# Optimization experiments

Measured on AMD Instinct MI355X. Metric: run time of the kernel, lower is better.

## Reference

```python
import jax, jax.numpy as jnp
import numpy as np

MUL = 64                  # multiplicity of 0e and 1o channels
N_NODES = 50000
N_EDGES = 500000
DIM_KEY = 32
FEAT = MUL * 4            # 64x0e (64) + 64x1o (192) = 256
# e3nn FullyConnectedTensorProduct(in, '10x0e', out) normalization:
# path_weight * w3j = 1/sqrt(mul_in * mul_z) = 1/sqrt(64*10)
INV640 = 1.0 / np.sqrt(MUL * 10)
ISQ3 = 1.0 / np.sqrt(3.0)   # w3j(1,1,0) = delta/sqrt(3)
ISQ2 = 1.0 / np.sqrt(2.0)   # path_weight sqrt(alpha) after 'element' norm (2 paths/out)


def _fctp(x, z, W0, W1):
    """FullyConnectedTensorProduct('64x0e+64x1o', '10x0e', '64x0e+64x1o').
    Scalars mix 0e block, vectors mix 1o block; w3j/path-weight factors reduce to 1/sqrt(640)."""
    x0 = x[:, :MUL]                       # (N, 64)
    x1 = x[:, MUL:].reshape(-1, MUL, 3)   # (N, 64, 3)
    o0 = jnp.einsum('nu,nv,uvw->nw', x0, z, W0) * INV640
    o1 = jnp.einsum('nuk,nv,uvw->nwk', x1, z, W1) * INV640
    return jnp.concatenate([o0, o1.reshape(-1, MUL * 3)], axis=-1)


def setup_inputs() -> dict:
    key = jax.random.key(0)
    ks = jax.random.split(key, 13)
    return {
        'x': jax.random.normal(ks[0], (N_NODES, FEAT), jnp.float32),
        'z': jax.random.normal(ks[1], (N_NODES, 10), jnp.float32),
        'edge_src': jax.random.randint(ks[2], (N_EDGES,), 0, N_NODES, jnp.int32),
        'edge_dst': jax.random.randint(ks[3], (N_EDGES,), 0, N_NODES, jnp.int32),
        'edge_len_emb': jax.random.normal(ks[4], (N_EDGES, DIM_KEY), jnp.float32),
        'edge_attr': jax.random.normal(ks[5], (N_EDGES, 4), jnp.float32),
        # learned params: four FCTPs (si, lin1, lin2 each have one 0e and one 1o path)
        'W_si0': jax.random.normal(ks[6], (MUL, 10, MUL), jnp.float32),
        'W_si1': jax.random.normal(ks[7], (MUL, 10, MUL), jnp.float32),
        'W_l1_0': jax.random.normal(ks[8], (MUL, 10, MUL), jnp.float32),
        'W_l1_1': jax.random.normal(ks[9], (MUL, 10, MUL), jnp.float32),
        'W_l2_0': jax.random.normal(ks[10], (MUL, 10, MUL), jnp.float32),
        'W_l2_1': jax.random.normal(ks[11], (MUL, 10, MUL), jnp.float32),
        # per-edge TP weights: 4 'uvu' paths x 64 = 256
        'tp_weight': jax.random.normal(ks[12], (DIM_KEY, 4 * MUL), jnp.float32),
    }


def reference(x, z, edge_src, edge_dst, edge_len_emb, edge_attr,
              W_si0, W_si1, W_l1_0, W_l1_1, W_l2_0, W_l2_1, tp_weight):
    n = x.shape[0]
    s = _fctp(x, z, W_si0, W_si1)          # self-interaction
    xl = _fctp(x, z, W_l1_0, W_l1_1)       # lin1

    w = edge_len_emb @ tp_weight           # (E, 256) per-edge TP weights
    w1, w2, w3, w4 = jnp.split(w, 4, axis=-1)  # instr order: 0ex0e->0e, 0ex1o->1o, 1ox0e->1o, 1ox1o->0e

    xs = xl[edge_src]                      # gather (E, 256)
    x0 = xs[:, :MUL]                       # (E, 64)
    x1 = xs[:, MUL:].reshape(-1, MUL, 3)   # (E, 64, 3)
    sh0 = edge_attr[:, 0:1]                # (E, 1) scalar SH
    sh1 = edge_attr[:, 1:4]                # (E, 3) vector SH

    # 'uvu' weighted tensor product (component norm, element path norm):
    # out_0e = sqrt(1/2) * [ w1*x0*sh0 + w4*(x1.sh1)/sqrt(3) ]
    e0 = ISQ2 * (w1 * x0 * sh0 + ISQ3 * w4 * jnp.einsum('euk,ek->eu', x1, sh1))
    # out_1o = sqrt(3/2)/sqrt(3) * [ w2*x0*sh1 + w3*x1*sh0 ]
    e1 = ISQ2 * (w2[:, :, None] * x0[:, :, None] * sh1[:, None, :]
                 + w3[:, :, None] * x1 * sh0[:, :, None])
    edge_out = jnp.concatenate([e0, e1.reshape(-1, MUL * 3)], axis=-1)  # (E, 256)

    # scatter-add messages to destination nodes
    agg = jnp.zeros((n, FEAT), edge_out.dtype).at[edge_dst].add(edge_out)

    x_out = _fctp(agg, z, W_l2_0, W_l2_1)  # lin2
    return s + x_out / 10
```

## Files before the change

### kernel.cpp

```cpp
#include <hip/hip_runtime.h>

#define MULT 64
#define FEATD 256
#define ZDIM 10

#define INV640f 0.03952847075210474f
#define ISQ2f   0.7071067811865476f
#define ISQ3f   0.5773502691896258f

typedef _Float16 f16_t;
typedef f16_t f16x8_t __attribute__((ext_vector_type(8)));
typedef f16_t f16x4_t __attribute__((ext_vector_type(4)));
typedef float f32x4_t __attribute__((ext_vector_type(4)));

__global__ __launch_bounds__(256) void transform_x2(
    const float* __restrict__ x, f16_t* __restrict__ Xs,
    f16_t* __restrict__ Xv, int N)
{
    int idx = blockIdx.x * 256 + threadIdx.x;
    if (idx >= N * MULT) return;
    int n = idx >> 6;
    int u = idx & 63;
    const float* row = x + (size_t)n * FEATD;
    Xs[idx] = (f16_t)row[u];
    const float* x1p = row + MULT + u * 3;
    Xv[((size_t)3 * n + 0) * MULT + u] = (f16_t)x1p[0];
    Xv[((size_t)3 * n + 1) * MULT + u] = (f16_t)x1p[1];
    Xv[((size_t)3 * n + 2) * MULT + u] = (f16_t)x1p[2];
}

__device__ __forceinline__ void preload_W(
    const float* __restrict__ W, int c0, int q, int mm, f16x8_t (&B)[20])
{
    const int col = c0 + mm;
#pragma unroll
    for (int ks = 0; ks < 20; ++ks) {
        const int v = ks >> 1;
        const int ub = ((ks & 1) << 5) + (q << 3);
        const int base = v * 64 + col;
#pragma unroll
        for (int j = 0; j < 8; ++j)
            B[ks][j] = (f16_t)W[(ub + j) * 640 + base];
    }
}

__global__ __launch_bounds__(256, 2) void fctp_stageA_mfma(
    const f16_t* __restrict__ Xs, const f16_t* __restrict__ Xv,
    const float* __restrict__ z,
    const float* __restrict__ Wsi0, const float* __restrict__ Wsi1,
    const float* __restrict__ Wl10, const float* __restrict__ Wl11,
    float* __restrict__ out, f16_t* __restrict__ xls,
    f16_t* __restrict__ xlv, int N)
{
    const int lane = threadIdx.x & 63;
    const int wave = threadIdx.x >> 6;
    const int c0 = wave << 4;
    const int q = lane >> 4;
    const int mm = lane & 15;
    const bool sc = (int)blockIdx.x < 128;
    const float* WA = sc ? Wsi0 : Wsi1;
    const float* WB = sc ? Wl10 : Wl11;
    const f16_t* Xsel = sc ? Xs : Xv;
    const int ntiles = sc ? (N >> 4) : ((3 * N) >> 4);
    const int worker = sc ? (int)blockIdx.x : ((int)blockIdx.x - 128);
    const int nworkers = sc ? 128 : 384;

    f16x8_t BA[20], BB[20];
    preload_W(WA, c0, q, mm, BA);
    preload_W(WB, c0, q, mm, BB);

    for (int tile = worker; tile < ntiles; tile += nworkers) {
        const int r = (tile << 4) + mm;
        f16x8_t xlo = *(const f16x8_t*)(Xsel + ((size_t)r << 6) + (q << 3));
        f16x8_t xhi = *(const f16x8_t*)(Xsel + ((size_t)r << 6) + 32 + (q << 3));
        float xf[16];
#pragma unroll
        for (int j = 0; j < 8; ++j) { xf[j] = (float)xlo[j]; xf[8 + j] = (float)xhi[j]; }
        const unsigned node = sc ? (unsigned)r : ((unsigned)r / 3u);
        float zr[ZDIM];
#pragma unroll
        for (int v = 0; v < ZDIM; ++v) zr[v] = z[(size_t)node * ZDIM + v] * INV640f;

        f32x4_t accA = {0.f, 0.f, 0.f, 0.f}, accB = {0.f, 0.f, 0.f, 0.f};
#pragma unroll
        for (int ks = 0; ks < 20; ++ks) {
            const float zv = zr[ks >> 1];
            const int xo = (ks & 1) << 3;
            f16x8_t af;
#pragma unroll
            for (int j = 0; j < 8; ++j) af[j] = (f16_t)(zv * xf[xo + j]);
            accA = __builtin_amdgcn_mfma_f32_16x16x32_f16(af, BA[ks], accA, 0, 0, 0);
            accB = __builtin_amdgcn_mfma_f32_16x16x32_f16(af, BB[ks], accB, 0, 0, 0);
        }

        const int w = c0 + mm;
        const int rb = (tile << 4) + (q << 2);
#pragma unroll
        for (int reg = 0; reg < 4; ++reg) {
            const int ro = rb + reg;
            if (sc) {
                out[(size_t)ro * FEATD + w] = accA[reg];
                xls[((size_t)ro << 6) + w] = (f16_t)accB[reg];
            } else {
                const unsigned nn = (unsigned)ro / 3u;
                const int k = ro - 3 * (int)nn;
                out[(size_t)nn * FEATD + MULT + w * 3 + k] = accA[reg];
                xlv[((size_t)ro << 6) + w] = (f16_t)accB[reg];
            }
        }
    }
}

__global__ __launch_bounds__(256, 2) void fctp_stageC_mfma(
    const float* __restrict__ aggs, const float* __restrict__ aggv,
    const float* __restrict__ z,
    const float* __restrict__ Wl20, const float* __restrict__ Wl21,
    float* __restrict__ out, int N)
{
    const int lane = threadIdx.x & 63;
    const int wave = threadIdx.x >> 6;
    const int c0 = wave << 4;
    const int q = lane >> 4;
    const int mm = lane & 15;
    const bool sc = (int)blockIdx.x < 128;
    const float* W = sc ? Wl20 : Wl21;
    const float* Asel = sc ? aggs : aggv;
    const int ntiles = sc ? (N >> 4) : ((3 * N) >> 4);
    const int worker = sc ? (int)blockIdx.x : ((int)blockIdx.x - 128);
    const int nworkers = sc ? 128 : 384;

    f16x8_t B[20];
    preload_W(W, c0, q, mm, B);

    for (int tile = worker; tile < ntiles; tile += nworkers) {
        const int r = (tile << 4) + mm;
        const float* ap = Asel + ((size_t)r << 6) + (q << 3);
        float4 l0 = *(const float4*)(ap);
        float4 l1 = *(const float4*)(ap + 4);
        float4 h0 = *(const float4*)(ap + 32);
        float4 h1 = *(const float4*)(ap + 36);
        float xf[16] = {l0.x, l0.y, l0.z, l0.w, l1.x, l1.y, l1.z, l1.w,
                        h0.x, h0.y, h0.z, h0.w, h1.x, h1.y, h1.z, h1.w};
        const unsigned node = sc ? (unsigned)r : ((unsigned)r / 3u);
        float zr[ZDIM];
#pragma unroll
        for (int v = 0; v < ZDIM; ++v)
            zr[v] = z[(size_t)node * ZDIM + v] * (INV640f * 0.1f);

        f32x4_t acc = {0.f, 0.f, 0.f, 0.f};
#pragma unroll
        for (int ks = 0; ks < 20; ++ks) {
            const float zv = zr[ks >> 1];
            const int xo = (ks & 1) << 3;
            f16x8_t af;
#pragma unroll
            for (int j = 0; j < 8; ++j) af[j] = (f16_t)(zv * xf[xo + j]);
            acc = __builtin_amdgcn_mfma_f32_16x16x32_f16(af, B[ks], acc, 0, 0, 0);
        }

        const int w = c0 + mm;
        const int rb = (tile << 4) + (q << 2);
#pragma unroll
        for (int reg = 0; reg < 4; ++reg) {
            const int ro = rb + reg;
            size_t idx;
            if (sc) {
                idx = (size_t)ro * FEATD + w;
            } else {
                const unsigned nn = (unsigned)ro / 3u;
                const int k = ro - 3 * (int)nn;
                idx = (size_t)nn * FEATD + MULT + w * 3 + k;
            }
            out[idx] = out[idx] + acc[reg];
        }
    }
}

__global__ __launch_bounds__(256) void hist_kernel(
    const int* __restrict__ edst, int* __restrict__ cnt, int E)
{
    int e = blockIdx.x * 256 + threadIdx.x;
    if (e >= E) return;
    atomicAdd(&cnt[edst[e]], 1);
}

__global__ __launch_bounds__(1024) void scan_block(
    const int* __restrict__ cnt, int* __restrict__ off,
    int* __restrict__ bsum, int N)
{
    __shared__ int sh[1024];
    int tid = threadIdx.x;
    int i = blockIdx.x * 1024 + tid;
    int v = (i < N) ? cnt[i] : 0;
    sh[tid] = v;
    __syncthreads();
#pragma unroll
    for (int d = 1; d < 1024; d <<= 1) {
        int t = (tid >= d) ? sh[tid - d] : 0;
        __syncthreads();
        sh[tid] += t;
        __syncthreads();
    }
    if (i < N) off[i + 1] = sh[tid];
    if (tid == 1023) bsum[blockIdx.x] = sh[1023];
    if (i == 0) off[0] = 0;
}

__global__ __launch_bounds__(64) void scan_sums(int* __restrict__ bsum, int nb)
{
    int tid = threadIdx.x;
    int v = (tid < nb) ? bsum[tid] : 0;
#pragma unroll
    for (int d = 1; d < 64; d <<= 1) {
        int t = __shfl_up(v, d, 64);
        if (tid >= d) v += t;
    }
    int ex = __shfl_up(v, 1, 64);
    if (tid == 0) ex = 0;
    if (tid < nb) bsum[tid] = ex;
}

__global__ __launch_bounds__(1024) void scan_add(
    int* __restrict__ off, const int* __restrict__ bsum, int N)
{
    int i = blockIdx.x * 1024 + threadIdx.x;
    if (i < N) off[i + 1] += bsum[blockIdx.x];
}

__global__ __launch_bounds__(256) void scatter_kernel(
    const int* __restrict__ edst, const int* __restrict__ esrc,
    const float* __restrict__ eattr, const int* __restrict__ off,
    int* __restrict__ cursor, int* __restrict__ perm,
    int* __restrict__ sperm, float* __restrict__ eattr_p, int E)
{
    int e = blockIdx.x * 256 + threadIdx.x;
    if (e >= E) return;
    int d = edst[e];
    int pos = off[d] + atomicAdd(&cursor[d], 1);
    perm[pos] = e;
    sperm[pos] = esrc[e];
    float4 at = *(const float4*)(eattr + (size_t)e * 4);
    *(float4*)(eattr_p + (size_t)pos * 4) = at;
}

__global__ __launch_bounds__(256, 2) void wgemm_kernel(
    const int* __restrict__ perm, const float* __restrict__ elem,
    const float* __restrict__ tpw, f16_t* __restrict__ wbuf,
    int lo, int ntiles)
{
    int tt = blockIdx.x * 4 + (threadIdx.x >> 6);
    if (tt >= ntiles) return;
    const int lane = threadIdx.x & 63;
    const int mm = lane & 15, q = lane >> 4;

    f16x8_t B[16];
#pragma unroll
    for (int s = 0; s < 16; ++s)
#pragma unroll
        for (int j = 0; j < 8; ++j)
            B[s][j] = (f16_t)tpw[(q * 8 + j) * 256 + s * 16 + mm];

    int p = lo + tt * 16 + mm;
    int e = perm[p];
    const float* er = elem + ((size_t)e << 5) + q * 8;
    float4 ea = *(const float4*)er;
    float4 eb = *(const float4*)(er + 4);
    f16x8_t A;
    A[0] = (f16_t)ea.x; A[1] = (f16_t)ea.y; A[2] = (f16_t)ea.z; A[3] = (f16_t)ea.w;
    A[4] = (f16_t)eb.x; A[5] = (f16_t)eb.y; A[6] = (f16_t)eb.z; A[7] = (f16_t)eb.w;

    f32x4_t D[16];
#pragma unroll
    for (int s = 0; s < 16; ++s) {
        f32x4_t zer = {0.f, 0.f, 0.f, 0.f};
        D[s] = __builtin_amdgcn_mfma_f32_16x16x32_f16(A, B[s], zer, 0, 0, 0);
    }

#pragma unroll
    for (int reg = 0; reg < 4; ++reg) {
        const int row = q * 4 + reg;
        const size_t base = ((size_t)(tt * 16 + row)) << 6;
#pragma unroll
        for (int t = 0; t < 4; ++t) {
            const int u = t * 16 + mm;
            f16x4_t wq;
            wq[0] = (f16_t)(D[0 * 4 + t][reg] * ISQ2f);
            wq[1] = (f16_t)(D[1 * 4 + t][reg] * ISQ2f);
            wq[2] = (f16_t)(D[2 * 4 + t][reg] * ISQ2f);
            wq[3] = (f16_t)(D[3 * 4 + t][reg] * (ISQ2f * ISQ3f));
            *(f16x4_t*)(wbuf + ((base + u) << 2)) = wq;
        }
    }
}

__device__ __forceinline__ void agg_edge5(
    float xs, float v0, float v1, float v2, int i, int lo,
    const f16_t* __restrict__ wbuf, const float* __restrict__ eattr_p, int u,
    float& accx, float& accy, float& accz, float& accw)
{
    f16x4_t wq = *(const f16x4_t*)(wbuf + ((((size_t)(i - lo)) << 6) + u) * 4);
    float w1 = (float)wq[0], w2 = (float)wq[1], w3 = (float)wq[2], w4 = (float)wq[3];
    float4 at = *(const float4*)(eattr_p + ((size_t)i << 2));
    float dot3 = v0 * at.y + v1 * at.z + v2 * at.w;
    accx = fmaf(w1 * xs, at.x, accx);
    accx = fmaf(w4, dot3, accx);
    float w2x = w2 * xs;
    accy = fmaf(w2x, at.y, accy);
    accz = fmaf(w2x, at.z, accz);
    accw = fmaf(w2x, at.w, accw);
    float w3s = w3 * at.x;
    accy = fmaf(w3s, v0, accy);
    accz = fmaf(w3s, v1, accz);
    accw = fmaf(w3s, v2, accw);
}

__global__ __launch_bounds__(256, 8) void aggregate5(
    const int* __restrict__ off, const int* __restrict__ sperm,
    const f16_t* __restrict__ wbuf, const float* __restrict__ eattr_p,
    const f16_t* __restrict__ xls, const f16_t* __restrict__ xlv,
    float* __restrict__ aggs, float* __restrict__ aggv,
    int N, int lo, int hi)
{
    int n = (blockIdx.x * 256 + threadIdx.x) >> 6;
    if (n >= N) return;
    int u = threadIdx.x & 63;

    int s0 = __builtin_amdgcn_readfirstlane(off[n]);
    int s1 = __builtin_amdgcn_readfirstlane(off[n + 1]);
    int cs0 = s0 > lo ? s0 : lo;
    int cs1 = s1 < hi ? s1 : hi;
    if (cs0 >= cs1) return;

    float accx = 0.f, accy = 0.f, accz = 0.f, accw = 0.f;
    const int last = cs1 - 1;

    int sa = __builtin_amdgcn_readfirstlane(sperm[cs0]);
    float a_xs = (float)xls[((size_t)sa << 6) + u];
    float a_v0 = (float)xlv[((size_t)(3 * sa + 0) << 6) + u];
    float a_v1 = (float)xlv[((size_t)(3 * sa + 1) << 6) + u];
    float a_v2 = (float)xlv[((size_t)(3 * sa + 2) << 6) + u];
    int ib = (cs0 + 1 <= last) ? cs0 + 1 : last;
    int sb = __builtin_amdgcn_readfirstlane(sperm[ib]);
    float b_xs = (float)xls[((size_t)sb << 6) + u];
    float b_v0 = (float)xlv[((size_t)(3 * sb + 0) << 6) + u];
    float b_v1 = (float)xlv[((size_t)(3 * sb + 1) << 6) + u];
    float b_v2 = (float)xlv[((size_t)(3 * sb + 2) << 6) + u];

    int i = cs0;
    while (true) {
        agg_edge5(a_xs, a_v0, a_v1, a_v2, i, lo, wbuf, eattr_p, u,
                  accx, accy, accz, accw);
        {
            int inx = (i + 2 <= last) ? i + 2 : last;
            int sn = __builtin_amdgcn_readfirstlane(sperm[inx]);
            a_xs = (float)xls[((size_t)sn << 6) + u];
            a_v0 = (float)xlv[((size_t)(3 * sn + 0) << 6) + u];
            a_v1 = (float)xlv[((size_t)(3 * sn + 1) << 6) + u];
            a_v2 = (float)xlv[((size_t)(3 * sn + 2) << 6) + u];
        }
        if (++i > last) break;
        agg_edge5(b_xs, b_v0, b_v1, b_v2, i, lo, wbuf, eattr_p, u,
                  accx, accy, accz, accw);
        {
            int inx = (i + 2 <= last) ? i + 2 : last;
            int sn = __builtin_amdgcn_readfirstlane(sperm[inx]);
            b_xs = (float)xls[((size_t)sn << 6) + u];
            b_v0 = (float)xlv[((size_t)(3 * sn + 0) << 6) + u];
            b_v1 = (float)xlv[((size_t)(3 * sn + 1) << 6) + u];
            b_v2 = (float)xlv[((size_t)(3 * sn + 2) << 6) + u];
        }
        if (++i > last) break;
    }

    aggs[((size_t)n << 6) + u] += accx;
    aggv[((size_t)(3 * n + 0) << 6) + u] += accy;
    aggv[((size_t)(3 * n + 1) << 6) + u] += accz;
    aggv[((size_t)(3 * n + 2) << 6) + u] += accw;
}

extern "C" void kernel_launch(void* const* d_in, const int* in_sizes, int n_in,
                              void* d_out, int out_size, void* d_ws, size_t ws_size,
                              hipStream_t stream)
{
    const float* x     = (const float*)d_in[0];
    const float* z     = (const float*)d_in[1];
    const int*   esrc  = (const int*)d_in[2];
    const int*   edst  = (const int*)d_in[3];
    const float* elem  = (const float*)d_in[4];
    const float* eattr = (const float*)d_in[5];
    const float* Wsi0  = (const float*)d_in[6];
    const float* Wsi1  = (const float*)d_in[7];
    const float* Wl10  = (const float*)d_in[8];
    const float* Wl11  = (const float*)d_in[9];
    const float* Wl20  = (const float*)d_in[10];
    const float* Wl21  = (const float*)d_in[11];
    const float* tpw   = (const float*)d_in[12];
    float* out = (float*)d_out;

    const int N = in_sizes[1] / ZDIM;
    const int E = in_sizes[2];
    const int Ehalf = E / 2;

    f16_t* xls  = (f16_t*)d_ws;
    f16_t* xlv  = xls + (size_t)N * 64;
    float* aggs = (float*)(xlv + (size_t)3 * N * 64);
    float* aggv = aggs + (size_t)N * 64;
    char*  R    = (char*)(aggv + (size_t)3 * N * 64);
    f16_t* Xs   = (f16_t*)R;
    f16_t* Xv   = Xs + (size_t)N * 64;
    f16_t* wbuf = (f16_t*)R;
    size_t Rbytes = (size_t)Ehalf * 256 * sizeof(f16_t);
    float* eattr_p = (float*)(R + Rbytes);
    int*   sperm   = (int*)(eattr_p + (size_t)E * 4);
    int*   perm    = sperm + E;
    int*   cnt     = perm + E;
    int*   cursor  = cnt + N;
    int*   off     = cursor + N;
    int*   bsum    = off + (N + 1);

    const int SCAN_B = 1024;
    int nb = (N + SCAN_B - 1) / SCAN_B;

    hipMemsetAsync(cnt, 0, 2 * (size_t)N * sizeof(int), stream);
    hipMemsetAsync(aggs, 0, (size_t)4 * N * 64 * sizeof(float), stream);

    int g0 = (N * MULT + 255) / 256;
    hipLaunchKernelGGL(transform_x2, dim3(g0), dim3(256), 0, stream, x, Xs, Xv, N);

    hipLaunchKernelGGL(fctp_stageA_mfma, dim3(512), dim3(256), 0, stream,
                       Xs, Xv, z, Wsi0, Wsi1, Wl10, Wl11, out, xls, xlv, N);

    int geh = (E + 255) / 256;
    hipLaunchKernelGGL(hist_kernel, dim3(geh), dim3(256), 0, stream,
                       edst, cnt, E);
    hipLaunchKernelGGL(scan_block, dim3(nb), dim3(SCAN_B), 0, stream,
                       cnt, off, bsum, N);
    hipLaunchKernelGGL(scan_sums, dim3(1), dim3(64), 0, stream, bsum, nb);
    hipLaunchKernelGGL(scan_add, dim3(nb), dim3(SCAN_B), 0, stream,
                       off, bsum, N);
    hipLaunchKernelGGL(scatter_kernel, dim3(geh), dim3(256), 0, stream,
                       edst, esrc, eattr, off, cursor, perm, sperm, eattr_p, E);

    int wt = Ehalf / 16;
    int gw = (wt + 3) / 4;
    int ga = (N * 64 + 255) / 256;
    for (int c = 0; c < 2; ++c) {
        int lo = c * Ehalf, hi = lo + Ehalf;
        hipLaunchKernelGGL(wgemm_kernel, dim3(gw), dim3(256), 0, stream,
                           perm, elem, tpw, wbuf, lo, wt);
        hipLaunchKernelGGL(aggregate5, dim3(ga), dim3(256), 0, stream,
                           off, sperm, wbuf, eattr_p, xls, xlv,
                           aggs, aggv, N, lo, hi);
    }

    hipLaunchKernelGGL(fctp_stageC_mfma, dim3(512), dim3(256), 0, stream,
                       aggs, aggv, z, Wl20, Wl21, out, N);
}
```

Before: 619.6 us.

## Factor z scaling out of FCTP MFMA inputs and precompute transposed z

Restructures the FCTP kernels so each z component scales the MFMA output (x·W_v) instead of scaling the f16 A-operand per k-step. This removes the per-element multiply and f16 conversions in the inner loop, at the cost of separate per-v accumulator MFMAs plus fma reductions. A new zprep kernel writes z pre-scaled and transposed, with a 3x replicated copy for vector rows, so the kernels can load it as vectors. Stage C's grid grows to 768 blocks. The changes add an extra kernel launch and workspace traffic, and precision behaviour shifts slightly.

```diff
diff --git a/kernel.cpp b/kernel.cpp
--- a/kernel.cpp
+++ b/kernel.cpp
@@ -29,6 +29,22 @@
     Xv[((size_t)3 * n + 2) * MULT + u] = (f16_t)x1p[2];
 }
 
+__global__ __launch_bounds__(256) void zprep_kernel(
+    const float* __restrict__ z, float* __restrict__ zt,
+    float* __restrict__ ztv, int N)
+{
+    int n = blockIdx.x * 256 + threadIdx.x;
+    if (n >= N) return;
+    const float* zr = z + (size_t)n * ZDIM;
+#pragma unroll
+    for (int v = 0; v < ZDIM; ++v) {
+        float val = zr[v] * INV640f;
+        zt[(size_t)v * N + n] = val;
+        float* p = ztv + (size_t)v * 3 * N + 3 * (size_t)n;
+        p[0] = val; p[1] = val; p[2] = val;
+    }
+}
+
 __device__ __forceinline__ void preload_W(
     const float* __restrict__ W, int c0, int q, int mm, f16x8_t (&B)[20])
 {
@@ -46,24 +62,26 @@
 
 __global__ __launch_bounds__(256, 2) void fctp_stageA_mfma(
     const f16_t* __restrict__ Xs, const f16_t* __restrict__ Xv,
-    const float* __restrict__ z,
+    const float* __restrict__ zt, const float* __restrict__ ztv,
     const float* __restrict__ Wsi0, const float* __restrict__ Wsi1,
     const float* __restrict__ Wl10, const float* __restrict__ Wl11,
     float* __restrict__ out, f16_t* __restrict__ xls,
-    f16_t* __restrict__ xlv, int N)
+    f16_t* __restrict__ xlv, int N, int nsc)
 {
     const int lane = threadIdx.x & 63;
     const int wave = threadIdx.x >> 6;
     const int c0 = wave << 4;
     const int q = lane >> 4;
     const int mm = lane & 15;
-    const bool sc = (int)blockIdx.x < 128;
+    const bool sc = (int)blockIdx.x < nsc;
     const float* WA = sc ? Wsi0 : Wsi1;
     const float* WB = sc ? Wl10 : Wl11;
     const f16_t* Xsel = sc ? Xs : Xv;
+    const float* ztb = sc ? zt : ztv;
+    const size_t zsr = sc ? (size_t)N : (size_t)3 * N;
     const int ntiles = sc ? (N >> 4) : ((3 * N) >> 4);
-    const int worker = sc ? (int)blockIdx.x : ((int)blockIdx.x - 128);
-    const int nworkers = sc ? 128 : 384;
+    const int worker = sc ? (int)blockIdx.x : ((int)blockIdx.x - nsc);
+    const int nworkers = sc ? nsc : 3 * nsc;
 
     f16x8_t BA[20], BB[20];
     preload_W(WA, c0, q, mm, BA);
@@ -73,31 +91,28 @@
         const int r = (tile << 4) + mm;
         f16x8_t xlo = *(const f16x8_t*)(Xsel + ((size_t)r << 6) + (q << 3));
         f16x8_t xhi = *(const f16x8_t*)(Xsel + ((size_t)r << 6) + 32 + (q << 3));
-        float xf[16];
-#pragma unroll
-        for (int j = 0; j < 8; ++j) { xf[j] = (float)xlo[j]; xf[8 + j] = (float)xhi[j]; }
-        const unsigned node = sc ? (unsigned)r : ((unsigned)r / 3u);
-        float zr[ZDIM];
-#pragma unroll
-        for (int v = 0; v < ZDIM; ++v) zr[v] = z[(size_t)node * ZDIM + v] * INV640f;
+        const int rb4 = (tile << 4) + (q << 2);
 
         f32x4_t accA = {0.f, 0.f, 0.f, 0.f}, accB = {0.f, 0.f, 0.f, 0.f};
 #pragma unroll
-        for (int ks = 0; ks < 20; ++ks) {
-            const float zv = zr[ks >> 1];
-            const int xo = (ks & 1) << 3;
-            f16x8_t af;
-#pragma unroll
-            for (int j = 0; j < 8; ++j) af[j] = (f16_t)(zv * xf[xo + j]);
-            accA = __builtin_amdgcn_mfma_f32_16x16x32_f16(af, BA[ks], accA, 0, 0, 0);
-            accB = __builtin_amdgcn_mfma_f32_16x16x32_f16(af, BB[ks], accB, 0, 0, 0);
+        for (int v = 0; v < ZDIM; ++v) {
+            f32x4_t tA = {0.f, 0.f, 0.f, 0.f}, tB = {0.f, 0.f, 0.f, 0.f};
+            tA = __builtin_amdgcn_mfma_f32_16x16x32_f16(xlo, BA[2 * v], tA, 0, 0, 0);
+            tA = __builtin_amdgcn_mfma_f32_16x16x32_f16(xhi, BA[2 * v + 1], tA, 0, 0, 0);
+            tB = __builtin_amdgcn_mfma_f32_16x16x32_f16(xlo, BB[2 * v], tB, 0, 0, 0);
+            tB = __builtin_amdgcn_mfma_f32_16x16x32_f16(xhi, BB[2 * v + 1], tB, 0, 0, 0);
+            f32x4_t zq = *(const f32x4_t*)(ztb + (size_t)v * zsr + rb4);
+#pragma unroll
+            for (int reg = 0; reg < 4; ++reg) {
+                accA[reg] = fmaf(zq[reg], tA[reg], accA[reg]);
+                accB[reg] = fmaf(zq[reg], tB[reg], accB[reg]);
+            }
         }
 
         const int w = c0 + mm;
-        const int rb = (tile << 4) + (q << 2);
 #pragma unroll
         for (int reg = 0; reg < 4; ++reg) {
-            const int ro = rb + reg;
+            const int ro = rb4 + reg;
             if (sc) {
                 out[(size_t)ro * FEATD + w] = accA[reg];
                 xls[((size_t)ro << 6) + w] = (f16_t)accB[reg];
@@ -113,21 +128,23 @@
 
 __global__ __launch_bounds__(256, 2) void fctp_stageC_mfma(
     const float* __restrict__ aggs, const float* __restrict__ aggv,
-    const float* __restrict__ z,
+    const float* __restrict__ zt, const float* __restrict__ ztv,
     const float* __restrict__ Wl20, const float* __restrict__ Wl21,
-    float* __restrict__ out, int N)
+    float* __restrict__ out, int N, int nsc)
 {
     const int lane = threadIdx.x & 63;
     const int wave = threadIdx.x >> 6;
     const int c0 = wave << 4;
     const int q = lane >> 4;
     const int mm = lane & 15;
-    const bool sc = (int)blockIdx.x < 128;
+    const bool sc = (int)blockIdx.x < nsc;
     const float* W = sc ? Wl20 : Wl21;
     const float* Asel = sc ? aggs : aggv;
+    const float* ztb = sc ? zt : ztv;
+    const size_t zsr = sc ? (size_t)N : (size_t)3 * N;
     const int ntiles = sc ? (N >> 4) : ((3 * N) >> 4);
-    const int worker = sc ? (int)blockIdx.x : ((int)blockIdx.x - 128);
-    const int nworkers = sc ? 128 : 384;
+    const int worker = sc ? (int)blockIdx.x : ((int)blockIdx.x - nsc);
+    const int nworkers = sc ? nsc : 3 * nsc;
 
     f16x8_t B[20];
     preload_W(W, c0, q, mm, B);
@@ -139,30 +156,29 @@
         float4 l1 = *(const float4*)(ap + 4);
         float4 h0 = *(const float4*)(ap + 32);
         float4 h1 = *(const float4*)(ap + 36);
-        float xf[16] = {l0.x, l0.y, l0.z, l0.w, l1.x, l1.y, l1.z, l1.w,
-                        h0.x, h0.y, h0.z, h0.w, h1.x, h1.y, h1.z, h1.w};
-        const unsigned node = sc ? (unsigned)r : ((unsigned)r / 3u);
-        float zr[ZDIM];
-#pragma unroll
-        for (int v = 0; v < ZDIM; ++v)
-            zr[v] = z[(size_t)node * ZDIM + v] * (INV640f * 0.1f);
+        f16x8_t xlo, xhi;
+        xlo[0] = (f16_t)l0.x; xlo[1] = (f16_t)l0.y; xlo[2] = (f16_t)l0.z; xlo[3] = (f16_t)l0.w;
+        xlo[4] = (f16_t)l1.x; xlo[5] = (f16_t)l1.y; xlo[6] = (f16_t)l1.z; xlo[7] = (f16_t)l1.w;
+        xhi[0] = (f16_t)h0.x; xhi[1] = (f16_t)h0.y; xhi[2] = (f16_t)h0.z; xhi[3] = (f16_t)h0.w;
+        xhi[4] = (f16_t)h1.x; xhi[5] = (f16_t)h1.y; xhi[6] = (f16_t)h1.z; xhi[7] = (f16_t)h1.w;
+        const int rb4 = (tile << 4) + (q << 2);
 
         f32x4_t acc = {0.f, 0.f, 0.f, 0.f};
 #pragma unroll
-        for (int ks = 0; ks < 20; ++ks) {
-            const float zv = zr[ks >> 1];
-            const int xo = (ks & 1) << 3;
-            f16x8_t af;
-#pragma unroll
-            for (int j = 0; j < 8; ++j) af[j] = (f16_t)(zv * xf[xo + j]);
-            acc = __builtin_amdgcn_mfma_f32_16x16x32_f16(af, B[ks], acc, 0, 0, 0);
+        for (int v = 0; v < ZDIM; ++v) {
+            f32x4_t t = {0.f, 0.f, 0.f, 0.f};
+            t = __builtin_amdgcn_mfma_f32_16x16x32_f16(xlo, B[2 * v], t, 0, 0, 0);
+            t = __builtin_amdgcn_mfma_f32_16x16x32_f16(xhi, B[2 * v + 1], t, 0, 0, 0);
+            f32x4_t zq = *(const f32x4_t*)(ztb + (size_t)v * zsr + rb4);
+#pragma unroll
+            for (int reg = 0; reg < 4; ++reg)
+                acc[reg] = fmaf(zq[reg], t[reg], acc[reg]);
         }
 
         const int w = c0 + mm;
-        const int rb = (tile << 4) + (q << 2);
 #pragma unroll
         for (int reg = 0; reg < 4; ++reg) {
-            const int ro = rb + reg;
+            const int ro = rb4 + reg;
             size_t idx;
             if (sc) {
                 idx = (size_t)ro * FEATD + w;
@@ -171,7 +187,7 @@
                 const int k = ro - 3 * (int)nn;
                 idx = (size_t)nn * FEATD + MULT + w * 3 + k;
             }
-            out[idx] = out[idx] + acc[reg];
+            out[idx] = out[idx] + acc[reg] * 0.1f;
         }
     }
 }
@@ -417,6 +433,9 @@
     int*   cursor  = cnt + N;
     int*   off     = cursor + N;
     int*   bsum    = off + (N + 1);
+    size_t zoff = (((size_t)(bsum + 64) - (size_t)d_ws) + 255) & ~(size_t)255;
+    float* zt  = (float*)((char*)d_ws + zoff);
+    float* ztv = zt + (size_t)10 * N;
 
     const int SCAN_B = 1024;
     int nb = (N + SCAN_B - 1) / SCAN_B;
@@ -426,9 +445,12 @@
 
     int g0 = (N * MULT + 255) / 256;
     hipLaunchKernelGGL(transform_x2, dim3(g0), dim3(256), 0, stream, x, Xs, Xv, N);
+    int gz = (N + 255) / 256;
+    hipLaunchKernelGGL(zprep_kernel, dim3(gz), dim3(256), 0, stream, z, zt, ztv, N);
 
     hipLaunchKernelGGL(fctp_stageA_mfma, dim3(512), dim3(256), 0, stream,
-                       Xs, Xv, z, Wsi0, Wsi1, Wl10, Wl11, out, xls, xlv, N);
+                       Xs, Xv, zt, ztv, Wsi0, Wsi1, Wl10, Wl11, out, xls, xlv,
+                       N, 128);
 
     int geh = (E + 255) / 256;
     hipLaunchKernelGGL(hist_kernel, dim3(geh), dim3(256), 0, stream,
@@ -453,6 +475,6 @@
                            aggs, aggv, N, lo, hi);
     }
 
-    hipLaunchKernelGGL(fctp_stageC_mfma, dim3(512), dim3(256), 0, stream,
-                       aggs, aggv, z, Wl20, Wl21, out, N);
-}
+    hipLaunchKernelGGL(fctp_stageC_mfma, dim3(768), dim3(256), 0, stream,
+                       aggs, aggv, zt, ztv, Wl20, Wl21, out, N, 192);
+}
```

Measured after the change: 680.6 us. +9.8%, slower.
